# Kernel tuning notes

Hardware: AMD Instinct MI355X
Metric: run time of the kernel (lower is better)

The kernel has to match this reference:

```python
import jax, jax.numpy as jnp
import numpy as np

B, T, D = 8, 8192, 256
H = 16            # history_length
K = 3             # neighbor kernel_size
DECAY = 0.9
EPS = 1e-5


def _layernorm(x, g, b):
    m = jnp.mean(x, axis=-1, keepdims=True)
    v = jnp.var(x, axis=-1, keepdims=True)
    return (x - m) * jax.lax.rsqrt(v + EPS) * g + b


def _window_weighted_sum(x_pad, weights, seq_len):
    # sum_j w[j] * x_pad[:, j:j+T, :] -- fixed-weight local aggregation,
    # avoids materializing the [B,T,W,D] unfold tensor.
    out = weights[0] * x_pad[:, 0:seq_len, :]
    for j in range(1, weights.shape[0]):
        out = out + weights[j] * x_pad[:, j:j + seq_len, :]
    return out


def temporal_weights():
    w = DECAY ** np.arange(H, dtype=np.float32)
    return jnp.asarray(w / w.sum())


def setup_inputs() -> dict:
    key = jax.random.key(0)
    ks = jax.random.split(key, 16)
    s = 1.0 / np.sqrt(D)
    s2 = 1.0 / np.sqrt(2 * D)
    inp = {
        "x": jax.random.normal(ks[0], (B, T, D), jnp.float32),
        # LayerNorms
        "n1_g": jnp.ones((D,), jnp.float32), "n1_b": jnp.zeros((D,), jnp.float32),
        "n2_g": jnp.ones((D,), jnp.float32), "n2_b": jnp.zeros((D,), jnp.float32),
        "n3_g": jnp.ones((D,), jnp.float32), "n3_b": jnp.zeros((D,), jnp.float32),
        # temporal value/out proj (stored as [in,out])
        "t_Wv": jax.random.uniform(ks[1], (D, D), jnp.float32, -s, s),
        "t_bv": jax.random.uniform(ks[2], (D,), jnp.float32, -s, s),
        "t_Wo": jax.random.uniform(ks[3], (D, D), jnp.float32, -s, s),
        "t_bo": jax.random.uniform(ks[4], (D,), jnp.float32, -s, s),
        # neighbor value/out proj
        "a_Wv": jax.random.uniform(ks[5], (D, D), jnp.float32, -s, s),
        "a_bv": jax.random.uniform(ks[6], (D,), jnp.float32, -s, s),
        "a_Wo": jax.random.uniform(ks[7], (D, D), jnp.float32, -s, s),
        "a_bo": jax.random.uniform(ks[8], (D,), jnp.float32, -s, s),
        # FFN
        "f_W1": jax.random.uniform(ks[9], (D, 2 * D), jnp.float32, -s, s),
        "f_b1": jax.random.uniform(ks[10], (2 * D,), jnp.float32, -s, s),
        "f_W2": jax.random.uniform(ks[11], (2 * D, D), jnp.float32, -s2, s2),
        "f_b2": jax.random.uniform(ks[12], (D,), jnp.float32, -s2, s2),
    }
    return inp


def reference(x, n1_g, n1_b, n2_g, n2_b, n3_g, n3_b,
              t_Wv, t_bv, t_Wo, t_bo,
              a_Wv, a_bv, a_Wo, a_bo,
              f_W1, f_b1, f_W2, f_b2):
    # --- temporal memory: causal fixed exponential-decay window ---
    h = _layernorm(x, n1_g, n1_b)
    h_pad = jnp.pad(h, ((0, 0), (H - 1, 0), (0, 0)))  # zeros on the left
    tw = temporal_weights()  # tw[j] weights the j-th-oldest element (decay^j)
    agg = _window_weighted_sum(h_pad, tw, T)
    # weights sum to 1 => weighted-sum-of-linear == linear-of-weighted-sum
    attended = agg @ t_Wv + t_bv
    x = x + (attended @ t_Wo + t_bo)

    # --- neighbor attention: [t-1, t, t+1] uniform window, replicate pad ---
    h = _layernorm(x, n2_g, n2_b)
    h_pad = jnp.pad(h, ((0, 0), (1, 1), (0, 0)), mode="edge")
    nw = jnp.full((K,), 1.0 / K, jnp.float32)
    agg = _window_weighted_sum(h_pad, nw, T)
    attended = agg @ a_Wv + a_bv
    x = x + (attended @ a_Wo + a_bo)

    # --- FFN (dropout is identity at eval) ---
    h = _layernorm(x, n3_g, n3_b)
    h = jax.nn.gelu(h @ f_W1 + f_b1, approximate=False)
    x = x + (h @ f_W2 + f_b2)
    return x
```

## Files before the change

### kernel.cpp

```cpp
#include <hip/hip_runtime.h>
#include <cstdint>
#include <cstddef>

#define TT 8192
#define BB 8
#define DD 256
#define NTOK (BB * TT)

typedef unsigned short u16;
typedef unsigned int u32;

typedef __attribute__((ext_vector_type(8))) short bf16x8;
typedef __attribute__((ext_vector_type(4))) float f32x4;

__device__ __forceinline__ float bf2f(u16 u) {
    u32 v = ((u32)u) << 16;
    float f;
    __builtin_memcpy(&f, &v, 4);
    return f;
}

__device__ __forceinline__ u16 f2bf(float f) {
    u32 v;
    __builtin_memcpy(&v, &f, 4);
    u32 r = (v + 0x7FFFu + ((v >> 16) & 1u)) >> 16;
    return (u16)r;
}

__device__ __forceinline__ uint2 pack4(const float* v) {
    uint2 p;
    p.x = (u32)f2bf(v[0]) | ((u32)f2bf(v[1]) << 16);
    p.y = (u32)f2bf(v[2]) | ((u32)f2bf(v[3]) << 16);
    return p;
}

__device__ __forceinline__ void unpack4(uint2 p, float* v) {
    v[0] = bf2f((u16)(p.x & 0xFFFFu));
    v[1] = bf2f((u16)(p.x >> 16));
    v[2] = bf2f((u16)(p.y & 0xFFFFu));
    v[3] = bf2f((u16)(p.y >> 16));
}

__device__ __forceinline__ uint4 pack8(const float* v) {
    uint4 p;
    p.x = (u32)f2bf(v[0]) | ((u32)f2bf(v[1]) << 16);
    p.y = (u32)f2bf(v[2]) | ((u32)f2bf(v[3]) << 16);
    p.z = (u32)f2bf(v[4]) | ((u32)f2bf(v[5]) << 16);
    p.w = (u32)f2bf(v[6]) | ((u32)f2bf(v[7]) << 16);
    return p;
}

__device__ __forceinline__ void unpack8(uint4 p, float* v) {
    v[0] = bf2f((u16)(p.x & 0xFFFFu));
    v[1] = bf2f((u16)(p.x >> 16));
    v[2] = bf2f((u16)(p.y & 0xFFFFu));
    v[3] = bf2f((u16)(p.y >> 16));
    v[4] = bf2f((u16)(p.z & 0xFFFFu));
    v[5] = bf2f((u16)(p.z >> 16));
    v[6] = bf2f((u16)(p.w & 0xFFFFu));
    v[7] = bf2f((u16)(p.w >> 16));
}

__global__ __launch_bounds__(256) void k_diag(float* out, float code) {
    out[(size_t)blockIdx.x * 256 + threadIdx.x] = code;
}

__global__ __launch_bounds__(256) void k_transpose(
    const float* s0, const float* s1, const float* s2, const float* s3,
    const float* s4, const float* s5,
    u16* d0, u16* d1, u16* d2, u16* d3, u16* d4, u16* d5,
    const float* tbv, const float* tbo, const float* abv, const float* abo,
    float* bc1, float* bc2) {
    const int z = blockIdx.z;
    if (z >= 6) {
        if (blockIdx.x || blockIdx.y) return;
        const float* bv = (z == 7) ? abv : tbv;
        const float* Wo = (z == 7) ? s1 : s0;
        const float* bo = (z == 7) ? abo : tbo;
        float* bc = (z == 7) ? bc2 : bc1;
        const int n = threadIdx.x;
        float s = bo[n];
        for (int j = 0; j < 256; j++) s += bv[j] * Wo[j * 256 + n];
        bc[n] = s;
        return;
    }
    const float* src;
    u16* dst;
    int K, N, tr;
    switch (z) {
        case 0: src = s0; dst = d0; K = 256; N = 256; tr = 1; break;
        case 1: src = s1; dst = d1; K = 256; N = 256; tr = 1; break;
        case 2: src = s2; dst = d2; K = 256; N = 512; tr = 1; break;
        case 3: src = s3; dst = d3; K = 512; N = 256; tr = 1; break;
        case 4: src = s4; dst = d4; K = 256; N = 256; tr = 0; break;
        default: src = s5; dst = d5; K = 256; N = 256; tr = 0; break;
    }
    const int nb = blockIdx.x * 32, kb = blockIdx.y * 32;
    if (nb >= N || kb >= K) return;
    const int tx = threadIdx.x & 31, ty = threadIdx.x >> 5;
    if (!tr) {
        for (int i = ty; i < 32; i += 8)
            dst[(size_t)(kb + i) * N + nb + tx] =
                f2bf(src[(size_t)(kb + i) * N + nb + tx]);
        return;
    }
    __shared__ u16 tile[32][33];
    for (int i = ty; i < 32; i += 8)
        tile[i][tx] = f2bf(src[(size_t)(kb + i) * N + nb + tx]);
    __syncthreads();
    for (int i = ty; i < 32; i += 8)
        dst[(size_t)(nb + i) * K + kb + tx] = tile[tx][i];
}

__global__ __launch_bounds__(256) void k_gemm_prep(
    const u16* __restrict__ A0, const u16* __restrict__ B0, u16* O0,
    const u16* __restrict__ A1, const u16* __restrict__ B1, u16* O1) {
    const u16* A = blockIdx.z ? A1 : A0;
    const u16* Wt = blockIdx.z ? B1 : B0;
    u16* out = blockIdx.z ? O1 : O0;
    const int m0 = blockIdx.y * 128;
    const int n0 = blockIdx.x * 128;
    const int tid = threadIdx.x;
    const int wv = tid >> 6, lane = tid & 63;
    const int quad = lane >> 4, l16 = lane & 15;
    const int wm = (wv >> 1) * 64, wn = (wv & 1) * 64;

    __shared__ u16 lA[128 * 40];
    __shared__ u16 lB[128 * 40];

    f32x4 acc[4][4];
#pragma unroll
    for (int i = 0; i < 4; i++)
#pragma unroll
        for (int j = 0; j < 4; j++) acc[i][j] = (f32x4){0.f, 0.f, 0.f, 0.f};

    const int r = tid >> 2;
    const int c = tid & 3;

    for (int k0 = 0; k0 < 256; k0 += 32) {
        __syncthreads();
        {
            const uint4 a0 = *(const uint4*)(A + (size_t)(m0 + r) * 256 + k0 + c * 8);
            const uint4 a1 = *(const uint4*)(A + (size_t)(m0 + r + 64) * 256 + k0 + c * 8);
            const uint4 b0 = *(const uint4*)(Wt + (size_t)(n0 + r) * 256 + k0 + c * 8);
            const uint4 b1 = *(const uint4*)(Wt + (size_t)(n0 + r + 64) * 256 + k0 + c * 8);
            *(uint4*)(lA + r * 40 + c * 8) = a0;
            *(uint4*)(lA + (r + 64) * 40 + c * 8) = a1;
            *(uint4*)(lB + r * 40 + c * 8) = b0;
            *(uint4*)(lB + (r + 64) * 40 + c * 8) = b1;
        }
        __syncthreads();
        bf16x8 af[4], bfr[4];
#pragma unroll
        for (int i = 0; i < 4; i++)
            af[i] = *(const bf16x8*)(lA + (wm + i * 16 + l16) * 40 + quad * 8);
#pragma unroll
        for (int j = 0; j < 4; j++)
            bfr[j] = *(const bf16x8*)(lB + (wn + j * 16 + l16) * 40 + quad * 8);
#pragma unroll
        for (int i = 0; i < 4; i++)
#pragma unroll
            for (int j = 0; j < 4; j++)
                acc[i][j] = __builtin_amdgcn_mfma_f32_16x16x32_bf16(
                    af[i], bfr[j], acc[i][j], 0, 0, 0);
    }

#pragma unroll
    for (int i = 0; i < 4; i++) {
        const int rowb = m0 + wm + i * 16 + quad * 4;
#pragma unroll
        for (int j = 0; j < 4; j++) {
            const int col = n0 + wn + j * 16 + l16;
#pragma unroll
            for (int rr = 0; rr < 4; rr++)
                out[(size_t)(rowb + rr) * 256 + col] = f2bf(acc[i][j][rr]);
        }
    }
}

__global__ __launch_bounds__(512, 4) void k_p12(
    const float* __restrict__ x, const float* __restrict__ n1g,
    const float* __restrict__ n1b, const u16* __restrict__ Wt,
    const float* __restrict__ bias, float* outf,
    const float* __restrict__ lng, const float* __restrict__ lnb,
    u16* __restrict__ hout) {
    const int b = blockIdx.y;
    const int t0 = blockIdx.x * 64;
    const size_t base = (size_t)b * TT;
    const int t = threadIdx.x;
    const int lane = t & 63, wv = t >> 6;
    const int quad = lane >> 4, l16 = lane & 15;
    const int wn = wv * 32;

    __shared__ __attribute__((aligned(16))) u16 hl[79 * 256];
    __shared__ __attribute__((aligned(16))) u16 sAg[64 * 264];
    float* sE = (float*)hl;
    __shared__ float sMean[16], sRstd[16];
    __shared__ float sG[256], sBl[256];

    if (t < 256) {
        sG[t] = lng[t];
        sBl[t] = lnb[t];
    }

    const int d4 = lane * 4;
    {
        const float4 gv = *(const float4*)(n1g + d4);
        const float4 bv = *(const float4*)(n1b + d4);
        for (int i = wv; i < 79; i += 8) {
            const int tt = t0 + i - 15;
            if (tt < 0) {
                *(uint2*)(hl + i * 256 + d4) = make_uint2(0u, 0u);
                continue;
            }
            const float4 v = *(const float4*)(x + (base + tt) * DD + d4);
            float s = v.x + v.y + v.z + v.w;
            float ss = v.x * v.x + v.y * v.y + v.z * v.z + v.w * v.w;
            for (int m = 1; m < 64; m <<= 1) {
                s += __shfl_xor(s, m);
                ss += __shfl_xor(ss, m);
            }
            const float mean = s * (1.0f / 256.0f);
            const float var = ss * (1.0f / 256.0f) - mean * mean;
            const float rs = rsqrtf(fmaxf(var, 0.f) + 1e-5f);
            float h[4] = {(v.x - mean) * rs * gv.x + bv.x,
                          (v.y - mean) * rs * gv.y + bv.y,
                          (v.z - mean) * rs * gv.z + bv.z,
                          (v.w - mean) * rs * gv.w + bv.w};
            *(uint2*)(hl + i * 256 + d4) = pack4(h);
        }
    }
    __syncthreads();

    {
        float p = 1.f, s = 0.f, w15 = 1.f;
        for (int j = 0; j < 16; j++) {
            s += p;
            if (j == 15) w15 = p;
            p *= 0.9f;
        }
        const float c = 1.f / s;
        const float inv09 = 1.0f / 0.9f;
        const int tg = wv * 8;
        float g[4] = {0.f, 0.f, 0.f, 0.f};
        float pw = 1.f;
        for (int j = 0; j < 16; j++) {
            float h[4];
            unpack4(*(const uint2*)(hl + (tg + j) * 256 + d4), h);
            g[0] += pw * h[0];
            g[1] += pw * h[1];
            g[2] += pw * h[2];
            g[3] += pw * h[3];
            pw *= 0.9f;
        }
        {
            float a[4] = {c * g[0], c * g[1], c * g[2], c * g[3]};
            *(uint2*)(sAg + tg * 264 + d4) = pack4(a);
        }
        for (int ot = tg + 1; ot < tg + 8; ++ot) {
            float hold[4], hnew[4];
            unpack4(*(const uint2*)(hl + (ot - 1) * 256 + d4), hold);
            unpack4(*(const uint2*)(hl + (ot + 15) * 256 + d4), hnew);
#pragma unroll
            for (int e = 0; e < 4; e++)
                g[e] = (g[e] - hold[e]) * inv09 + w15 * hnew[e];
            float a[4] = {c * g[0], c * g[1], c * g[2], c * g[3]};
            *(uint2*)(sAg + ot * 264 + d4) = pack4(a);
        }
    }
    __syncthreads();

    f32x4 acc[4][2];
#pragma unroll
    for (int i = 0; i < 4; i++)
#pragma unroll
        for (int j = 0; j < 2; j++) acc[i][j] = (f32x4){0.f, 0.f, 0.f, 0.f};
#pragma unroll
    for (int ks = 0; ks < 8; ks++) {
        bf16x8 bfr[2], af[4];
#pragma unroll
        for (int j = 0; j < 2; j++)
            bfr[j] = *(const bf16x8*)(Wt + (size_t)(wn + j * 16 + l16) * 256 +
                                      ks * 32 + quad * 8);
#pragma unroll
        for (int i = 0; i < 4; i++)
            af[i] = *(const bf16x8*)(sAg + (i * 16 + l16) * 264 + ks * 32 +
                                     quad * 8);
#pragma unroll
        for (int i = 0; i < 4; i++)
#pragma unroll
            for (int j = 0; j < 2; j++)
                acc[i][j] = __builtin_amdgcn_mfma_f32_16x16x32_bf16(
                    af[i], bfr[j], acc[i][j], 0, 0, 0);
    }

    float bvl[2];
#pragma unroll
    for (int j = 0; j < 2; j++) bvl[j] = bias[wn + j * 16 + l16];

    const int row = t >> 5;
    const int colb = (t & 31) * 8;
    for (int cch = 0; cch < 4; cch++) {
        const size_t grow = base + t0 + cch * 16 + row;
        __syncthreads();
        {
            const float* rp = x + grow * 256 + colb;
            float* sp = sE + row * 268 + colb;
#pragma unroll
            for (int q = 0; q < 2; q++)
                *(float4*)(sp + q * 4) = *(const float4*)(rp + q * 4);
        }
        __syncthreads();
#pragma unroll
        for (int j = 0; j < 2; j++) {
#pragma unroll
            for (int rr = 0; rr < 4; rr++) {
                const int rl = quad * 4 + rr;
                const int ad = rl * 268 + wn + j * 16 + l16;
                sE[ad] += acc[cch][j][rr] + bvl[j];
            }
        }
        __syncthreads();
#pragma unroll
        for (int r4 = 0; r4 < 2; r4++) {
            const int rl = wv * 2 + r4;
            const float4 vv = *(const float4*)(sE + rl * 268 + lane * 4);
            float s = vv.x + vv.y + vv.z + vv.w;
            float ss = vv.x * vv.x + vv.y * vv.y + vv.z * vv.z + vv.w * vv.w;
            for (int m = 1; m < 64; m <<= 1) {
                s += __shfl_xor(s, m);
                ss += __shfl_xor(ss, m);
            }
            if (lane == 0) {
                const float mean = s * (1.0f / 256.0f);
                const float var = ss * (1.0f / 256.0f) - mean * mean;
                sMean[rl] = mean;
                sRstd[rl] = rsqrtf(fmaxf(var, 0.f) + 1e-5f);
            }
        }
        __syncthreads();
        const float* sp = sE + row * 268 + colb;
        {
            float* op = outf + grow * 256 + colb;
#pragma unroll
            for (int q = 0; q < 2; q++)
                *(float4*)(op + q * 4) = *(const float4*)(sp + q * 4);
        }
        {
            const float m = sMean[row], rs = sRstd[row];
            float h[8];
#pragma unroll
            for (int e = 0; e < 8; e++)
                h[e] = (sp[e] - m) * rs * sG[colb + e] + sBl[colb + e];
            u16* hp = hout + grow * 256 + colb;
            *(uint4*)hp = pack8(h);
        }
    }
}

__global__ __launch_bounds__(512, 4) void k_mega2(
    const u16* __restrict__ A,
    const u16* __restrict__ Wt,
    const float* __restrict__ bias,
    const float* res,
    float* outf,
    const float* __restrict__ lng, const float* __restrict__ lnb,
    u16* __restrict__ hout) {
    const int m0 = blockIdx.x * 64;
    const int t = threadIdx.x;
    const int lane = t & 63, wv = t >> 6;
    const int quad = lane >> 4, l16 = lane & 15;
    const int wn = wv * 32;

    __shared__ __attribute__((aligned(16))) u16 sA[8 * 64 * 40];
    float* sE = (float*)sA;
    __shared__ float sMean[16], sRstd[16];
    __shared__ float sG[256], sBl[256];

    if (t < 256) {
        sG[t] = lng[t];
        sBl[t] = lnb[t];
    }

#pragma unroll
    for (int q = 0; q < 4; q++) {
        const int id = q * 512 + t;
        const int arow = id >> 5;
        const int c8 = (id & 31) * 8;
        const int ks = c8 >> 5;
        const int kc = c8 & 31;
        const int gr = m0 + arow;
        const int rm = ((gr & (TT - 1)) == 0) ? gr : gr - 1;
        const int rp = (((gr + 1) & (TT - 1)) == 0) ? gr : gr + 1;
        float v0[8], v1[8], v2[8], o[8];
        unpack8(*(const uint4*)(A + (size_t)rm * 256 + c8), v0);
        unpack8(*(const uint4*)(A + (size_t)gr * 256 + c8), v1);
        unpack8(*(const uint4*)(A + (size_t)rp * 256 + c8), v2);
#pragma unroll
        for (int e = 0; e < 8; e++)
            o[e] = (v0[e] + v1[e] + v2[e]) * (1.0f / 3.0f);
        *(uint4*)(sA + (ks * 64 + arow) * 40 + kc) = pack8(o);
    }

    f32x4 acc[4][2];
#pragma unroll
    for (int i = 0; i < 4; i++)
#pragma unroll
        for (int j = 0; j < 2; j++) acc[i][j] = (f32x4){0.f, 0.f, 0.f, 0.f};

    __syncthreads();

#pragma unroll
    for (int ks = 0; ks < 8; ks++) {
        bf16x8 bfr[2], af[4];
#pragma unroll
        for (int j = 0; j < 2; j++)
            bfr[j] = *(const bf16x8*)(Wt + (size_t)(wn + j * 16 + l16) * 256 +
                                      ks * 32 + quad * 8);
#pragma unroll
        for (int i = 0; i < 4; i++)
            af[i] = *(const bf16x8*)(sA + (ks * 64 + i * 16 + l16) * 40 +
                                     quad * 8);
#pragma unroll
        for (int i = 0; i < 4; i++)
#pragma unroll
            for (int j = 0; j < 2; j++)
                acc[i][j] = __builtin_amdgcn_mfma_f32_16x16x32_bf16(
                    af[i], bfr[j], acc[i][j], 0, 0, 0);
    }

    float bvl[2];
#pragma unroll
    for (int j = 0; j < 2; j++) bvl[j] = bias[wn + j * 16 + l16];

    const int row = t >> 5;
    const int colb = (t & 31) * 8;
    for (int cch = 0; cch < 4; cch++) {
        const int gr = m0 + cch * 16 + row;
        __syncthreads();
        {
            const float* rp = res + (size_t)gr * 256 + colb;
            float* sp = sE + row * 268 + colb;
#pragma unroll
            for (int q = 0; q < 2; q++)
                *(float4*)(sp + q * 4) = *(const float4*)(rp + q * 4);
        }
        __syncthreads();
#pragma unroll
        for (int j = 0; j < 2; j++) {
#pragma unroll
            for (int rr = 0; rr < 4; rr++) {
                const int rl = quad * 4 + rr;
                const int ad = rl * 268 + wn + j * 16 + l16;
                sE[ad] += acc[cch][j][rr] + bvl[j];
            }
        }
        __syncthreads();
#pragma unroll
        for (int r4 = 0; r4 < 2; r4++) {
            const int rl = wv * 2 + r4;
            const float4 vv = *(const float4*)(sE + rl * 268 + lane * 4);
            float s = vv.x + vv.y + vv.z + vv.w;
            float ss = vv.x * vv.x + vv.y * vv.y + vv.z * vv.z + vv.w * vv.w;
            for (int m = 1; m < 64; m <<= 1) {
                s += __shfl_xor(s, m);
                ss += __shfl_xor(ss, m);
            }
            if (lane == 0) {
                const float mean = s * (1.0f / 256.0f);
                const float var = ss * (1.0f / 256.0f) - mean * mean;
                sMean[rl] = mean;
                sRstd[rl] = rsqrtf(fmaxf(var, 0.f) + 1e-5f);
            }
        }
        __syncthreads();
        const float* sp = sE + row * 268 + colb;
        {
            float* op = outf + (size_t)gr * 256 + colb;
#pragma unroll
            for (int q = 0; q < 2; q++)
                *(float4*)(op + q * 4) = *(const float4*)(sp + q * 4);
        }
        {
            const float m = sMean[row], rs = sRstd[row];
            float h[8];
#pragma unroll
            for (int e = 0; e < 8; e++)
                h[e] = (sp[e] - m) * rs * sG[colb + e] + sBl[colb + e];
            u16* hp = hout + (size_t)gr * 256 + colb;
            *(uint4*)hp = pack8(h);
        }
    }
}

__global__ __launch_bounds__(512, 4) void k_ffn(
    const u16* __restrict__ A,
    const u16* __restrict__ W1T,
    const float* __restrict__ b1,
    const u16* __restrict__ W2T,
    const float* __restrict__ b2,
    const float* res,
    float* out) {
    const int m0 = blockIdx.x * 64;
    const int t = threadIdx.x;
    const int lane = t & 63, wv = t >> 6;
    const int quad = lane >> 4, l16 = lane & 15;
    const int wn = wv * 32;

    __shared__ __attribute__((aligned(16))) u16 sA[8 * 64 * 40];
    __shared__ __attribute__((aligned(16))) u16 sT[64 * 136];
    float* sE = (float*)sA;

#pragma unroll
    for (int q = 0; q < 4; q++) {
        const int id = q * 512 + t;
        const int arow = id >> 5;
        const int c8 = (id & 31) * 8;
        const int ks = c8 >> 5;
        const int kc = c8 & 31;
        *(uint4*)(sA + (ks * 64 + arow) * 40 + kc) =
            *(const uint4*)(A + (size_t)(m0 + arow) * 256 + c8);
    }

    f32x4 acc2[4][2];
#pragma unroll
    for (int i = 0; i < 4; i++)
#pragma unroll
        for (int jj = 0; jj < 2; jj++) acc2[i][jj] = (f32x4){0.f, 0.f, 0.f, 0.f};

    __syncthreads();

    for (int j4 = 0; j4 < 4; j4++) {
        const int n1 = j4 * 128 + wv * 16 + l16;
        bf16x8 bw[8];
#pragma unroll
        for (int ks = 0; ks < 8; ks++)
            bw[ks] = *(const bf16x8*)(W1T + (size_t)n1 * 256 + ks * 32 + quad * 8);
        f32x4 acc1[4];
#pragma unroll
        for (int i = 0; i < 4; i++) acc1[i] = (f32x4){0.f, 0.f, 0.f, 0.f};
#pragma unroll
        for (int ks = 0; ks < 8; ks++) {
#pragma unroll
            for (int i = 0; i < 4; i++) {
                const bf16x8 af = *(const bf16x8*)(
                    sA + (ks * 64 + i * 16 + l16) * 40 + quad * 8);
                acc1[i] = __builtin_amdgcn_mfma_f32_16x16x32_bf16(
                    af, bw[ks], acc1[i], 0, 0, 0);
            }
        }
        bf16x8 bw2[8];
#pragma unroll
        for (int kh = 0; kh < 4; kh++)
#pragma unroll
            for (int jj = 0; jj < 2; jj++)
                bw2[kh * 2 + jj] = *(const bf16x8*)(
                    W2T + (size_t)(wn + jj * 16 + l16) * 512 + j4 * 128 +
                    kh * 32 + quad * 8);
        const float b1l = b1[n1];
#pragma unroll
        for (int i = 0; i < 4; i++)
#pragma unroll
            for (int rr = 0; rr < 4; rr++) {
                float v = acc1[i][rr] + b1l;
                v = 0.5f * v * (1.0f + erff(v * 0.70710678118654752f));
                sT[(i * 16 + quad * 4 + rr) * 136 + wv * 16 + l16] = f2bf(v);
            }
        __syncthreads();
#pragma unroll
        for (int kh = 0; kh < 4; kh++) {
#pragma unroll
            for (int i = 0; i < 4; i++) {
                const bf16x8 af = *(const bf16x8*)(
                    sT + (i * 16 + l16) * 136 + kh * 32 + quad * 8);
#pragma unroll
                for (int jj = 0; jj < 2; jj++)
                    acc2[i][jj] = __builtin_amdgcn_mfma_f32_16x16x32_bf16(
                        af, bw2[kh * 2 + jj], acc2[i][jj], 0, 0, 0);
            }
        }
        __syncthreads();
    }

    float bvl[2];
#pragma unroll
    for (int jj = 0; jj < 2; jj++) bvl[jj] = b2[wn + jj * 16 + l16];
    const int row = t >> 5;
    const int colb = (t & 31) * 8;
    for (int cch = 0; cch < 4; cch++) {
        const int gr = m0 + cch * 16 + row;
        __syncthreads();
        {
            const float* rp = res + (size_t)gr * 256 + colb;
            float* sp = sE + row * 268 + colb;
#pragma unroll
            for (int q = 0; q < 2; q++)
                *(float4*)(sp + q * 4) = *(const float4*)(rp + q * 4);
        }
        __syncthreads();
#pragma unroll
        for (int jj = 0; jj < 2; jj++)
#pragma unroll
            for (int rr = 0; rr < 4; rr++) {
                const int ad = (quad * 4 + rr) * 268 + wn + jj * 16 + l16;
                sE[ad] += acc2[cch][jj][rr] + bvl[jj];
            }
        __syncthreads();
        {
            float* op = out + (size_t)gr * 256 + colb;
            const float* sp = sE + row * 268 + colb;
#pragma unroll
            for (int q = 0; q < 2; q++)
                *(float4*)(op + q * 4) = *(const float4*)(sp + q * 4);
        }
    }
}

extern "C" void kernel_launch(void* const* d_in, const int* in_sizes, int n_in,
                              void* d_out, int out_size, void* d_ws,
                              size_t ws_size, hipStream_t stream) {
    const float* x = (const float*)d_in[0];
    const float* n1g = (const float*)d_in[1];
    const float* n1b = (const float*)d_in[2];
    const float* n2g = (const float*)d_in[3];
    const float* n2b = (const float*)d_in[4];
    const float* n3g = (const float*)d_in[5];
    const float* n3b = (const float*)d_in[6];
    const float* tWv = (const float*)d_in[7];
    const float* tbv = (const float*)d_in[8];
    const float* tWo = (const float*)d_in[9];
    const float* tbo = (const float*)d_in[10];
    const float* aWv = (const float*)d_in[11];
    const float* abv = (const float*)d_in[12];
    const float* aWo = (const float*)d_in[13];
    const float* abo = (const float*)d_in[14];
    const float* fW1 = (const float*)d_in[15];
    const float* fb1 = (const float*)d_in[16];
    const float* fW2 = (const float*)d_in[17];
    const float* fb2 = (const float*)d_in[18];
    float* outp = (float*)d_out;

    u16* wq = (u16*)d_ws;
    u16* tWoT = wq;
    u16* aWoT = wq + 65536;
    u16* fW1T = wq + 131072;
    u16* fW2T = wq + 262144;
    u16* WcT1 = wq + 393216;
    u16* WcT2 = wq + 458752;
    u16* tWvB = wq + 524288;
    u16* aWvB = wq + 589824;
    float* bc1 = (float*)(wq + 655360);
    float* bc2 = (float*)(wq + 655872);
    const size_t W_ELEMS = 656384;
    const size_t SLOT = (size_t)NTOK * 256;
    u16* slot1 = wq + W_ELEMS;
    u16* slot2 = slot1 + SLOT;

    const size_t need = (W_ELEMS + 3 * SLOT) * 2;
    if (ws_size < need) {
        k_diag<<<dim3(NTOK), 256, 0, stream>>>(outp,
                                               512.0f + (float)(ws_size >> 20));
        return;
    }

    k_transpose<<<dim3(16, 16, 8), 256, 0, stream>>>(
        tWo, aWo, fW1, fW2, tWv, aWv, tWoT, aWoT, fW1T, fW2T, tWvB, aWvB,
        tbv, tbo, abv, abo, bc1, bc2);
    k_gemm_prep<<<dim3(2, 2, 2), 256, 0, stream>>>(tWoT, tWvB, WcT1, aWoT,
                                                   aWvB, WcT2);

    k_p12<<<dim3(TT / 64, BB), 512, 0, stream>>>(x, n1g, n1b, WcT1, bc1, outp,
                                                 n2g, n2b, slot2);

    k_mega2<<<dim3(NTOK / 64), 512, 0, stream>>>(slot2, WcT2, bc2, outp, outp,
                                                 n3g, n3b, slot1);

    k_ffn<<<dim3(NTOK / 64), 512, 0, stream>>>(slot1, fW1T, fb1, fW2T, fb2,
                                               outp, outp);
}
```

Before: 336.0 us.

## Software-pipeline FFN GEMM1 with double-buffered GELU tile and wider epilogue chunks

The FFN kernel now double-buffers the GELU intermediate tile in shared memory and issues the next chunk's first GEMM before running the current chunk's second GEMM. This removes one barrier per iteration and lets the two matrix phases overlap. The residual epilogue now handles 32 rows per pass instead of 16, which halves the number of barrier-separated passes. The extra accumulators that stay live and the larger shared buffer could raise register and LDS pressure, which may lower occupancy under the 512x4 launch bounds.

```diff
diff --git a/kernel.cpp b/kernel.cpp
--- a/kernel.cpp
+++ b/kernel.cpp
@@ -493,6 +493,31 @@
     }
 }
 
+__device__ __forceinline__ void ffn_gemm1(
+    const u16* __restrict__ sA, const u16* __restrict__ W1T, int j4, int wv,
+    int l16, int quad, f32x4* acc1) {
+    const int n1 = j4 * 128 + wv * 16 + l16;
+#pragma unroll
+    for (int i = 0; i < 4; i++) acc1[i] = (f32x4){0.f, 0.f, 0.f, 0.f};
+#pragma unroll
+    for (int ksg = 0; ksg < 2; ksg++) {
+        bf16x8 bw[4];
+#pragma unroll
+        for (int k = 0; k < 4; k++)
+            bw[k] = *(const bf16x8*)(W1T + (size_t)n1 * 256 +
+                                     (ksg * 4 + k) * 32 + quad * 8);
+#pragma unroll
+        for (int k = 0; k < 4; k++)
+#pragma unroll
+            for (int i = 0; i < 4; i++) {
+                const bf16x8 af = *(const bf16x8*)(
+                    sA + ((ksg * 4 + k) * 64 + i * 16 + l16) * 40 + quad * 8);
+                acc1[i] = __builtin_amdgcn_mfma_f32_16x16x32_bf16(
+                    af, bw[k], acc1[i], 0, 0, 0);
+            }
+    }
+}
+
 __global__ __launch_bounds__(512, 4) void k_ffn(
     const u16* __restrict__ A,
     const u16* __restrict__ W1T,
@@ -508,7 +533,7 @@
     const int wn = wv * 32;
 
     __shared__ __attribute__((aligned(16))) u16 sA[8 * 64 * 40];
-    __shared__ __attribute__((aligned(16))) u16 sT[64 * 136];
+    __shared__ __attribute__((aligned(16))) u16 sT[2][64 * 136];
     float* sE = (float*)sA;
 
 #pragma unroll
@@ -530,25 +555,22 @@
 
     __syncthreads();
 
+    f32x4 acc1[4];
+    ffn_gemm1(sA, W1T, 0, wv, l16, quad, acc1);
+
+#pragma unroll
     for (int j4 = 0; j4 < 4; j4++) {
-        const int n1 = j4 * 128 + wv * 16 + l16;
-        bf16x8 bw[8];
-#pragma unroll
-        for (int ks = 0; ks < 8; ks++)
-            bw[ks] = *(const bf16x8*)(W1T + (size_t)n1 * 256 + ks * 32 + quad * 8);
-        f32x4 acc1[4];
-#pragma unroll
-        for (int i = 0; i < 4; i++) acc1[i] = (f32x4){0.f, 0.f, 0.f, 0.f};
-#pragma unroll
-        for (int ks = 0; ks < 8; ks++) {
-#pragma unroll
-            for (int i = 0; i < 4; i++) {
-                const bf16x8 af = *(const bf16x8*)(
-                    sA + (ks * 64 + i * 16 + l16) * 40 + quad * 8);
-                acc1[i] = __builtin_amdgcn_mfma_f32_16x16x32_bf16(
-                    af, bw[ks], acc1[i], 0, 0, 0);
-            }
-        }
+        u16* sTc = sT[j4 & 1];
+        const float b1l = b1[j4 * 128 + wv * 16 + l16];
+#pragma unroll
+        for (int i = 0; i < 4; i++)
+#pragma unroll
+            for (int rr = 0; rr < 4; rr++) {
+                float v = acc1[i][rr] + b1l;
+                v = 0.5f * v * (1.0f + erff(v * 0.70710678118654752f));
+                sTc[(i * 16 + quad * 4 + rr) * 136 + wv * 16 + l16] = f2bf(v);
+            }
+        __syncthreads();
         bf16x8 bw2[8];
 #pragma unroll
         for (int kh = 0; kh < 4; kh++)
@@ -557,60 +579,53 @@
                 bw2[kh * 2 + jj] = *(const bf16x8*)(
                     W2T + (size_t)(wn + jj * 16 + l16) * 512 + j4 * 128 +
                     kh * 32 + quad * 8);
-        const float b1l = b1[n1];
-#pragma unroll
-        for (int i = 0; i < 4; i++)
-#pragma unroll
-            for (int rr = 0; rr < 4; rr++) {
-                float v = acc1[i][rr] + b1l;
-                v = 0.5f * v * (1.0f + erff(v * 0.70710678118654752f));
-                sT[(i * 16 + quad * 4 + rr) * 136 + wv * 16 + l16] = f2bf(v);
-            }
-        __syncthreads();
+        if (j4 < 3) ffn_gemm1(sA, W1T, j4 + 1, wv, l16, quad, acc1);
 #pragma unroll
         for (int kh = 0; kh < 4; kh++) {
 #pragma unroll
             for (int i = 0; i < 4; i++) {
                 const bf16x8 af = *(const bf16x8*)(
-                    sT + (i * 16 + l16) * 136 + kh * 32 + quad * 8);
+                    sTc + (i * 16 + l16) * 136 + kh * 32 + quad * 8);
 #pragma unroll
                 for (int jj = 0; jj < 2; jj++)
                     acc2[i][jj] = __builtin_amdgcn_mfma_f32_16x16x32_bf16(
                         af, bw2[kh * 2 + jj], acc2[i][jj], 0, 0, 0);
             }
         }
-        __syncthreads();
     }
 
     float bvl[2];
 #pragma unroll
     for (int jj = 0; jj < 2; jj++) bvl[jj] = b2[wn + jj * 16 + l16];
-    const int row = t >> 5;
-    const int colb = (t & 31) * 8;
-    for (int cch = 0; cch < 4; cch++) {
-        const int gr = m0 + cch * 16 + row;
-        __syncthreads();
-        {
-            const float* rp = res + (size_t)gr * 256 + colb;
+    const int row = t >> 4;
+    const int colb = (t & 15) * 16;
+    for (int cch = 0; cch < 2; cch++) {
+        const int gr0 = m0 + cch * 32 + row;
+        __syncthreads();
+        {
+            const float* rp = res + (size_t)gr0 * 256 + colb;
             float* sp = sE + row * 268 + colb;
 #pragma unroll
-            for (int q = 0; q < 2; q++)
+            for (int q = 0; q < 4; q++)
                 *(float4*)(sp + q * 4) = *(const float4*)(rp + q * 4);
         }
         __syncthreads();
 #pragma unroll
-        for (int jj = 0; jj < 2; jj++)
-#pragma unroll
-            for (int rr = 0; rr < 4; rr++) {
-                const int ad = (quad * 4 + rr) * 268 + wn + jj * 16 + l16;
-                sE[ad] += acc2[cch][jj][rr] + bvl[jj];
-            }
-        __syncthreads();
-        {
-            float* op = out + (size_t)gr * 256 + colb;
+        for (int il = 0; il < 2; il++)
+#pragma unroll
+            for (int jj = 0; jj < 2; jj++)
+#pragma unroll
+                for (int rr = 0; rr < 4; rr++) {
+                    const int ad =
+                        (il * 16 + quad * 4 + rr) * 268 + wn + jj * 16 + l16;
+                    sE[ad] += acc2[cch * 2 + il][jj][rr] + bvl[jj];
+                }
+        __syncthreads();
+        {
+            float* op = out + (size_t)gr0 * 256 + colb;
             const float* sp = sE + row * 268 + colb;
 #pragma unroll
-            for (int q = 0; q < 2; q++)
+            for (int q = 0; q < 4; q++)
                 *(float4*)(op + q * 4) = *(const float4*)(sp + q * 4);
         }
     }
```

New measurement: 346.2 us. 3.1% more time.
